# Optimization experiments

Hardware: AMD Instinct MI355X
Metric: run time of the kernel (lower is better)

The kernel has to match this reference:

```python
import jax, jax.numpy as jnp
import numpy as np

B, C, H, W = 16, 3, 1024, 1024
DENSITY = 0.015
SIGMA = 1.5
K = 5  # blur kernel size
N_FLAKES = int(H * W * DENSITY)  # 15728


def setup_inputs() -> dict:
    key = jax.random.key(0)
    kx, ky, kxs, kr = jax.random.split(key, 4)
    x = jax.random.uniform(kx, (B, C, H, W), dtype=jnp.float32)
    ys = jax.random.randint(ky, (B, N_FLAKES), 0, H, dtype=jnp.int32)
    xs = jax.random.randint(kxs, (B, N_FLAKES), 0, W, dtype=jnp.int32)
    rs = jax.random.randint(kr, (B, N_FLAKES), 1, 4, dtype=jnp.int32)  # radius in {1,2,3}
    return {"x": x, "ys": ys, "xs": xs, "rs": rs}


def reference(x, ys, xs, rs):
    Bb, Cc, Hh, Ww = x.shape
    # --- vectorized flake stamping (replaces per-flake Python loop) ---
    # Each flake writes a (2r+1)x(2r+1) square of 0.95, clipped to image bounds.
    # Max radius is 3 -> enumerate the 7x7 = 49 candidate offsets per flake.
    off = jnp.arange(-3, 4)
    dyg, dxg = jnp.meshgrid(off, off, indexing="ij")
    dy = dyg.reshape(-1)  # [49]
    dx = dxg.reshape(-1)  # [49]
    r = rs[..., None]  # [B, N, 1]
    valid = (jnp.abs(dy) <= r) & (jnp.abs(dx) <= r)  # [B, N, 49]
    # Clamping out-of-bounds coords to the border is equivalent to torch's
    # slice-clipping because the written value is a constant (0.95) and the
    # border pixel is already covered by an in-range offset. Invalid offsets
    # (|d| > r) are redirected to the flake center, which is always stamped.
    yy = jnp.where(valid, jnp.clip(ys[..., None] + dy, 0, Hh - 1), ys[..., None])
    xx = jnp.where(valid, jnp.clip(xs[..., None] + dx, 0, Ww - 1), xs[..., None])
    b = jnp.arange(Bb)[:, None, None]  # [B,1,1]
    out = x.at[b, :, yy, xx].set(0.95)  # stamp all channels

    # --- depthwise 5x5 gaussian blur ---
    coords = jnp.arange(K, dtype=jnp.float32) - K // 2
    g = jnp.exp(-(coords ** 2) / (2.0 * SIGMA ** 2))
    g = g / g.sum()
    kern = jnp.outer(g, g).astype(x.dtype)[None, None]  # [1,1,5,5]
    kern = jnp.broadcast_to(kern, (Cc, 1, K, K))  # depthwise: O=C, I=1
    pad = K // 2
    out = jax.lax.conv_general_dilated(
        out, kern, window_strides=(1, 1), padding=[(pad, pad), (pad, pad)],
        feature_group_count=Cc, dimension_numbers=("NCHW", "OIHW", "NCHW"))
    return jnp.clip(out, 0.0, 1.0)
```

## Files before the change

### kernel.cpp

```cpp
#include <hip/hip_runtime.h>


#define H_ 1024
#define W_ 1024
#define B_ 16
#define C_ 3
#define NF_ 15728
#define MASK_WORDS_PER_B (H_ * W_ / 32)

#define G0 0.12007838f
#define G1 0.23388076f
#define G2 0.29208172f

__global__ void clear_mask_kernel(uint4* __restrict__ mask, int n4) {
    int i = blockIdx.x * blockDim.x + threadIdx.x;
    if (i < n4) mask[i] = make_uint4(0u, 0u, 0u, 0u);
}

__global__ void stamp_kernel(const int* __restrict__ ys, const int* __restrict__ xs,
                             const int* __restrict__ rs, unsigned int* __restrict__ mask) {
    int t = blockIdx.x * blockDim.x + threadIdx.x;
    if (t >= B_ * NF_) return;
    int b = t / NF_;
    int y0 = ys[t], x0 = xs[t], r = rs[t];
    unsigned int* mb = mask + b * MASK_WORDS_PER_B;
    int xlo = max(x0 - r, 0), xhi = min(x0 + r, W_ - 1);
    int ylo = max(y0 - r, 0), yhi = min(y0 + r, H_ - 1);
    for (int y = ylo; y <= yhi; ++y) {
        int i0 = (y << 10) + xlo;
        int i1 = (y << 10) + xhi;
        int w0 = i0 >> 5, w1 = i1 >> 5;
        unsigned int m0 = ~0u << (i0 & 31);
        unsigned int m1 = ~0u >> (31 - (i1 & 31));
        if (w0 == w1) {
            atomicOr(mb + w0, m0 & m1);
        } else {
            atomicOr(mb + w0, m0);
            atomicOr(mb + w1, m1);
        }
    }
}

constexpr int TW = 128;
constexpr int TH = 32;

__global__ __launch_bounds__(256) void blur_kernel(const float* __restrict__ x,
                                                   const unsigned int* __restrict__ mask,
                                                   float* __restrict__ out) {
    int plane = blockIdx.z;
    int b = plane / C_;
    const float* xp = x + (size_t)plane * (H_ * W_);
    float* op = out + (size_t)plane * (H_ * W_);
    const unsigned int* mb = mask + b * MASK_WORDS_PER_B;

    const int tx0 = blockIdx.x * TW;
    const int ty0 = blockIdx.y * TH;
    const int tid = threadIdx.x;

    __shared__ float4 sin4[TH + 4][34];
    __shared__ float4 smid4[TH + 4][32];
    __shared__ unsigned int mrow[TH + 4][6];

    const int w0 = (tx0 >> 5) - 1;
    for (int i = tid; i < (TH + 4) * 6; i += 256) {
        int r = i / 6, w = i % 6;
        int gy = ty0 + r - 2;
        int cw = w0 + w;
        unsigned int m = 0u;
        if ((unsigned)gy < (unsigned)H_ && (unsigned)cw < (unsigned)(W_ / 32))
            m = mb[(gy << 5) + cw];
        mrow[r][w] = m;
    }
    __syncthreads();

    for (int i = tid; i < (TH + 4) * 34; i += 256) {
        int r = i / 34, j = i % 34;
        int gy = ty0 + r - 2;
        int gx4 = tx0 - 4 + 4 * j;
        float4 v = make_float4(0.f, 0.f, 0.f, 0.f);
        if ((unsigned)gy < (unsigned)H_ && (unsigned)gx4 < (unsigned)W_) {
            v = *(const float4*)(xp + (gy << 10) + gx4);
            unsigned int mw = mrow[r][(gx4 - tx0 + 32) >> 5];
            int bit = gx4 & 31;
            if ((mw >> (bit + 0)) & 1u) v.x = 0.95f;
            if ((mw >> (bit + 1)) & 1u) v.y = 0.95f;
            if ((mw >> (bit + 2)) & 1u) v.z = 0.95f;
            if ((mw >> (bit + 3)) & 1u) v.w = 0.95f;
        }
        sin4[r][j] = v;
    }
    __syncthreads();

    for (int i = tid; i < (TH + 4) * 32; i += 256) {
        int r = i >> 5;
        int j = i & 31;
        float2 A = *(const float2*)((const float*)&sin4[r][j] + 2);
        float4 Bv = sin4[r][j + 1];
        float2 Cv = *(const float2*)((const float*)&sin4[r][j + 2]);
        float4 o;
        o.x = G0 * (A.x  + Bv.z) + G1 * (A.y  + Bv.y) + G2 * Bv.x;
        o.y = G0 * (A.y  + Bv.w) + G1 * (Bv.x + Bv.z) + G2 * Bv.y;
        o.z = G0 * (Bv.x + Cv.x) + G1 * (Bv.y + Bv.w) + G2 * Bv.z;
        o.w = G0 * (Bv.y + Cv.y) + G1 * (Bv.z + Cv.x) + G2 * Bv.w;
        smid4[r][j] = o;
    }
    __syncthreads();

    for (int i = tid; i < TH * 32; i += 256) {
        int rr = i >> 5;
        int j = i & 31;
        float4 a0 = smid4[rr][j];
        float4 a1 = smid4[rr + 1][j];
        float4 a2 = smid4[rr + 2][j];
        float4 a3 = smid4[rr + 3][j];
        float4 a4 = smid4[rr + 4][j];
        float4 o;
        o.x = G0 * (a0.x + a4.x) + G1 * (a1.x + a3.x) + G2 * a2.x;
        o.y = G0 * (a0.y + a4.y) + G1 * (a1.y + a3.y) + G2 * a2.y;
        o.z = G0 * (a0.z + a4.z) + G1 * (a1.z + a3.z) + G2 * a2.z;
        o.w = G0 * (a0.w + a4.w) + G1 * (a1.w + a3.w) + G2 * a2.w;
        o.x = fminf(fmaxf(o.x, 0.0f), 1.0f);
        o.y = fminf(fmaxf(o.y, 0.0f), 1.0f);
        o.z = fminf(fmaxf(o.z, 0.0f), 1.0f);
        o.w = fminf(fmaxf(o.w, 0.0f), 1.0f);
        *(float4*)(op + ((ty0 + rr) << 10) + tx0 + 4 * j) = o;
    }
}

extern "C" void kernel_launch(void* const* d_in, const int* in_sizes, int n_in,
                              void* d_out, int out_size, void* d_ws, size_t ws_size,
                              hipStream_t stream) {
    const float* x  = (const float*)d_in[0];
    const int*   ys = (const int*)d_in[1];
    const int*   xs = (const int*)d_in[2];
    const int*   rs = (const int*)d_in[3];
    float* out = (float*)d_out;
    unsigned int* mask = (unsigned int*)d_ws;

    int n4 = B_ * MASK_WORDS_PER_B / 4;
    clear_mask_kernel<<<dim3((n4 + 255) / 256), dim3(256), 0, stream>>>((uint4*)mask, n4);

    int nst = B_ * NF_;
    stamp_kernel<<<dim3((nst + 255) / 256), dim3(256), 0, stream>>>(ys, xs, rs, mask);

    dim3 grid(W_ / TW, H_ / TH, B_ * C_);
    blur_kernel<<<grid, dim3(256), 0, stream>>>(x, mask, out);
}
```

Before: 405.2 us.

## Do vertical blur pass straight from global memory, horizontal pass from shared

The separable blur is reordered so each thread first computes the vertical 5-tap sum by reading five input rows (and their mask words) directly from global memory. The result goes into a single shared tile, and the horizontal pass runs from shared memory. This removes two shared staging buffers and two barriers, which lowers LDS usage and may raise occupancy. In exchange, each input element is fetched from global/L2 about five times instead of once per tile, which leans on the cache.

```diff
diff --git a/kernel.cpp b/kernel.cpp
--- a/kernel.cpp
+++ b/kernel.cpp
@@ -57,68 +57,50 @@
     const int ty0 = blockIdx.y * TH;
     const int tid = threadIdx.x;
 
-    __shared__ float4 sin4[TH + 4][34];
-    __shared__ float4 smid4[TH + 4][32];
-    __shared__ unsigned int mrow[TH + 4][6];
+    __shared__ float4 smid[TH][35];
 
-    const int w0 = (tx0 >> 5) - 1;
-    for (int i = tid; i < (TH + 4) * 6; i += 256) {
-        int r = i / 6, w = i % 6;
-        int gy = ty0 + r - 2;
-        int cw = w0 + w;
-        unsigned int m = 0u;
-        if ((unsigned)gy < (unsigned)H_ && (unsigned)cw < (unsigned)(W_ / 32))
-            m = mb[(gy << 5) + cw];
-        mrow[r][w] = m;
-    }
-    __syncthreads();
-
-    for (int i = tid; i < (TH + 4) * 34; i += 256) {
-        int r = i / 34, j = i % 34;
-        int gy = ty0 + r - 2;
+    for (int i = tid; i < TH * 34; i += 256) {
+        int r = i / 34;
+        int j = i - 34 * r;
         int gx4 = tx0 - 4 + 4 * j;
-        float4 v = make_float4(0.f, 0.f, 0.f, 0.f);
-        if ((unsigned)gy < (unsigned)H_ && (unsigned)gx4 < (unsigned)W_) {
-            v = *(const float4*)(xp + (gy << 10) + gx4);
-            unsigned int mw = mrow[r][(gx4 - tx0 + 32) >> 5];
+        float4 acc = make_float4(0.f, 0.f, 0.f, 0.f);
+        if ((unsigned)gx4 < (unsigned)W_) {
+            int cw = gx4 >> 5;
             int bit = gx4 & 31;
-            if ((mw >> (bit + 0)) & 1u) v.x = 0.95f;
-            if ((mw >> (bit + 1)) & 1u) v.y = 0.95f;
-            if ((mw >> (bit + 2)) & 1u) v.z = 0.95f;
-            if ((mw >> (bit + 3)) & 1u) v.w = 0.95f;
+            int gy0 = ty0 + r - 2;
+            #pragma unroll
+            for (int k = 0; k < 5; ++k) {
+                const float wk = (k == 0 || k == 4) ? G0 : ((k == 1 || k == 3) ? G1 : G2);
+                int gy = gy0 + k;
+                if ((unsigned)gy < (unsigned)H_) {
+                    float4 v = *(const float4*)(xp + (gy << 10) + gx4);
+                    unsigned int mw = mb[(gy << 5) + cw];
+                    if ((mw >> (bit + 0)) & 1u) v.x = 0.95f;
+                    if ((mw >> (bit + 1)) & 1u) v.y = 0.95f;
+                    if ((mw >> (bit + 2)) & 1u) v.z = 0.95f;
+                    if ((mw >> (bit + 3)) & 1u) v.w = 0.95f;
+                    acc.x += wk * v.x;
+                    acc.y += wk * v.y;
+                    acc.z += wk * v.z;
+                    acc.w += wk * v.w;
+                }
+            }
         }
-        sin4[r][j] = v;
-    }
-    __syncthreads();
-
-    for (int i = tid; i < (TH + 4) * 32; i += 256) {
-        int r = i >> 5;
-        int j = i & 31;
-        float2 A = *(const float2*)((const float*)&sin4[r][j] + 2);
-        float4 Bv = sin4[r][j + 1];
-        float2 Cv = *(const float2*)((const float*)&sin4[r][j + 2]);
-        float4 o;
-        o.x = G0 * (A.x  + Bv.z) + G1 * (A.y  + Bv.y) + G2 * Bv.x;
-        o.y = G0 * (A.y  + Bv.w) + G1 * (Bv.x + Bv.z) + G2 * Bv.y;
-        o.z = G0 * (Bv.x + Cv.x) + G1 * (Bv.y + Bv.w) + G2 * Bv.z;
-        o.w = G0 * (Bv.y + Cv.y) + G1 * (Bv.z + Cv.x) + G2 * Bv.w;
-        smid4[r][j] = o;
+        smid[r][j] = acc;
     }
     __syncthreads();
 
     for (int i = tid; i < TH * 32; i += 256) {
         int rr = i >> 5;
         int j = i & 31;
-        float4 a0 = smid4[rr][j];
-        float4 a1 = smid4[rr + 1][j];
-        float4 a2 = smid4[rr + 2][j];
-        float4 a3 = smid4[rr + 3][j];
-        float4 a4 = smid4[rr + 4][j];
+        float2 A  = *(const float2*)((const float*)&smid[rr][j] + 2);
+        float4 Bv = smid[rr][j + 1];
+        float2 Cv = *(const float2*)((const float*)&smid[rr][j + 2]);
         float4 o;
-        o.x = G0 * (a0.x + a4.x) + G1 * (a1.x + a3.x) + G2 * a2.x;
-        o.y = G0 * (a0.y + a4.y) + G1 * (a1.y + a3.y) + G2 * a2.y;
-        o.z = G0 * (a0.z + a4.z) + G1 * (a1.z + a3.z) + G2 * a2.z;
-        o.w = G0 * (a0.w + a4.w) + G1 * (a1.w + a3.w) + G2 * a2.w;
+        o.x = G0 * (A.x  + Bv.z) + G1 * (A.y  + Bv.y) + G2 * Bv.x;
+        o.y = G0 * (A.y  + Bv.w) + G1 * (Bv.x + Bv.z) + G2 * Bv.y;
+        o.z = G0 * (Bv.x + Cv.x) + G1 * (Bv.y + Bv.w) + G2 * Bv.z;
+        o.w = G0 * (Bv.y + Cv.y) + G1 * (Bv.z + Cv.x) + G2 * Bv.w;
         o.x = fminf(fmaxf(o.x, 0.0f), 1.0f);
         o.y = fminf(fmaxf(o.y, 0.0f), 1.0f);
         o.z = fminf(fmaxf(o.z, 0.0f), 1.0f);
```

New measurement: 484.2 us. 19.5% more time.
